# Optimization experiments

Hardware: AMD Instinct MI355X
Metric: run time of the kernel (lower is better)

## Reference

```python
import jax, jax.numpy as jnp
import numpy as np

B, T, D = 4, 2048, 1024
H, DH = 16, 64

def setup_inputs() -> dict:
    key = jax.random.key(0)
    k1, k2, k3 = jax.random.split(key, 3)
    x = jax.random.normal(k1, (B, T, D), dtype=jnp.float32)
    # nn.Linear weights stored [out, in]; we keep that convention
    w_attn = jax.random.normal(k2, (3 * D, D), dtype=jnp.float32) * (1.0 / np.sqrt(D))
    w_proj = jax.random.normal(k3, (D, D), dtype=jnp.float32) * (1.0 / np.sqrt(D))
    return {"x": x, "w_attn": w_attn, "w_proj": w_proj}

def reference(x, w_attn, w_proj):
    Bx, Tx, Dx = x.shape
    qkv = jnp.einsum('btd,ed->bte', x, w_attn)            # [B,T,3D]
    qkv = qkv.reshape(Bx, Tx, 3, H, DH)
    q = qkv[:, :, 0].transpose(0, 2, 1, 3)                # [B,H,T,DH]
    k = qkv[:, :, 1].transpose(0, 2, 1, 3)
    v = qkv[:, :, 2].transpose(0, 2, 1, 3)
    scale = 1.0 / np.sqrt(DH).astype(np.float32)
    att = jnp.einsum('bhqd,bhkd->bhqk', q, k) * scale     # [B,H,T,T]
    causal = jnp.tril(jnp.ones((Tx, Tx), dtype=bool))
    att = jnp.where(causal[None, None], att, jnp.float32(-jnp.inf))
    att = jax.nn.softmax(att, axis=-1)
    y = jnp.einsum('bhqk,bhkd->bhqd', att, v)             # [B,H,T,DH]
    y = y.transpose(0, 2, 1, 3).reshape(Bx, Tx, Dx)       # [B,T,D]
    y = jnp.einsum('btd,ed->bte', y, w_proj)
    return y
```

## Files before the change

### kernel.cpp

```cpp
#include <hip/hip_runtime.h>

typedef unsigned short u16;
typedef __bf16 bf16x8 __attribute__((ext_vector_type(8)));
typedef float floatx4 __attribute__((ext_vector_type(4)));
typedef u16 u16x4 __attribute__((ext_vector_type(4)));

__device__ inline u16 f2bf(float x) {
    __bf16 b = (__bf16)x;
    return __builtin_bit_cast(u16, b);
}

__device__ inline floatx4 fzero() {
    floatx4 z = {0.f, 0.f, 0.f, 0.f};
    return z;
}

#if defined(__has_builtin)
#if __has_builtin(__builtin_amdgcn_exp2f)
#define EXP2F(x) __builtin_amdgcn_exp2f(x)
#endif
#endif
#ifndef EXP2F
#define EXP2F(x) exp2f(x)
#endif

template <bool F32>
__device__ inline bf16x8 ld8(const void* base, size_t off) {
    if constexpr (F32) {
        const float* p = (const float*)base + off;
        float4 a = *(const float4*)p;
        float4 b = *(const float4*)(p + 4);
        union { u16 u[8]; bf16x8 v; } t;
        t.u[0] = f2bf(a.x); t.u[1] = f2bf(a.y); t.u[2] = f2bf(a.z); t.u[3] = f2bf(a.w);
        t.u[4] = f2bf(b.x); t.u[5] = f2bf(b.y); t.u[6] = f2bf(b.z); t.u[7] = f2bf(b.w);
        return t.v;
    } else {
        return *(const bf16x8*)((const u16*)base + off);
    }
}

typedef __attribute__((address_space(1))) const unsigned int as1_u32;
typedef __attribute__((address_space(3))) unsigned int as3_u32;
__device__ inline void gld_lds16(const void* g, void* l) {
    __builtin_amdgcn_global_load_lds((as1_u32*)g, (as3_u32*)l, 16, 0, 0);
}

__device__ inline u16* swz_ptr(u16* buf, int row, int col) {
    return (u16*)((char*)buf + row * 128 + ((col * 2) ^ ((row & 7) << 4)));
}

__global__ __launch_bounds__(256) void cvt_all(const float* __restrict__ x,
                                               const float* __restrict__ wa,
                                               const float* __restrict__ wp,
                                               u16* __restrict__ dst) {
    const int XB8 = 1048576, WAB8 = 393216;
    int i = blockIdx.x * 256 + threadIdx.x;
    const float* src; size_t off;
    if (i < XB8)             { src = x;  off = (size_t)i * 8; }
    else if (i < XB8 + WAB8) { src = wa; off = (size_t)(i - XB8) * 8; }
    else                     { src = wp; off = (size_t)(i - XB8 - WAB8) * 8; }
    *(bf16x8*)(dst + (size_t)i * 8) = ld8<true>(src, off);
}

#define BK 32

template <bool AF32, bool BF32, bool CF32, bool WVT>
__global__ __launch_bounds__(256) void gemm_bt(const void* __restrict__ Ap,
                                               const void* __restrict__ Bp,
                                               void* __restrict__ Cp,
                                               u16* __restrict__ vtp,
                                               int M, int N, int K) {
    __shared__ alignas(16) u16 As[2][128 * BK];
    __shared__ alignas(16) u16 Bs[2][128 * BK];

    const int tid  = threadIdx.x;
    const int lane = tid & 63;
    const int wave = tid >> 6;
    const int wm = (wave >> 1) * 64;
    const int wn = (wave & 1) * 64;
    const int tm = blockIdx.y * 128;
    const int tn = blockIdx.x * 128;
    const int l15 = lane & 15;
    const int l4  = lane >> 4;

    const int srow = tid >> 2;
    const int scol = (tid & 3) * 8;

    floatx4 acc[4][4];
#pragma unroll
    for (int i = 0; i < 4; i++)
#pragma unroll
        for (int j = 0; j < 4; j++) acc[i][j] = fzero();

    if constexpr (!AF32 && !BF32) {
        const u16* Ag = (const u16*)Ap + (size_t)(tm + srow) * K + scol;
        const u16* Bg = (const u16*)Bp + (size_t)(tn + srow) * K + scol;

        auto stage = [&](int buf, int k0) {
            gld_lds16(Ag + k0,                  &As[buf][wave * 512]);
            gld_lds16(Ag + k0 + (size_t)64 * K, &As[buf][2048 + wave * 512]);
            gld_lds16(Bg + k0,                  &Bs[buf][wave * 512]);
            gld_lds16(Bg + k0 + (size_t)64 * K, &Bs[buf][2048 + wave * 512]);
        };

        stage(0, 0);
        __syncthreads();
        int cur = 0;
        const int nk = K / BK;
        for (int t = 0; t < nk; t++) {
            if (t + 1 < nk) stage(cur ^ 1, (t + 1) * BK);

            bf16x8 af[4], bfv[4];
#pragma unroll
            for (int i = 0; i < 4; i++)
                af[i] = *(const bf16x8*)&As[cur][(wm + i * 16 + l15) * BK + l4 * 8];
#pragma unroll
            for (int j = 0; j < 4; j++)
                bfv[j] = *(const bf16x8*)&Bs[cur][(wn + j * 16 + l15) * BK + l4 * 8];
#pragma unroll
            for (int i = 0; i < 4; i++)
#pragma unroll
                for (int j = 0; j < 4; j++)
                    acc[i][j] = __builtin_amdgcn_mfma_f32_16x16x32_bf16(af[i], bfv[j], acc[i][j], 0, 0, 0);

            __syncthreads();
            cur ^= 1;
        }
    } else {
        for (int k0 = 0; k0 < K; k0 += BK) {
            bf16x8 av[2], bv[2];
#pragma unroll
            for (int q = 0; q < 2; q++) {
                av[q] = ld8<AF32>(Ap, (size_t)(tm + srow + q * 64) * K + k0 + scol);
                bv[q] = ld8<BF32>(Bp, (size_t)(tn + srow + q * 64) * K + k0 + scol);
            }
            __syncthreads();
#pragma unroll
            for (int q = 0; q < 2; q++) {
                *(bf16x8*)&As[0][(srow + q * 64) * BK + scol] = av[q];
                *(bf16x8*)&Bs[0][(srow + q * 64) * BK + scol] = bv[q];
            }
            __syncthreads();

            bf16x8 af[4], bfv[4];
#pragma unroll
            for (int i = 0; i < 4; i++)
                af[i] = *(const bf16x8*)&As[0][(wm + i * 16 + l15) * BK + l4 * 8];
#pragma unroll
            for (int j = 0; j < 4; j++)
                bfv[j] = *(const bf16x8*)&Bs[0][(wn + j * 16 + l15) * BK + l4 * 8];
#pragma unroll
            for (int i = 0; i < 4; i++)
#pragma unroll
                for (int j = 0; j < 4; j++)
                    acc[i][j] = __builtin_amdgcn_mfma_f32_16x16x32_bf16(af[i], bfv[j], acc[i][j], 0, 0, 0);
        }
    }

#pragma unroll
    for (int i = 0; i < 4; i++)
#pragma unroll
        for (int j = 0; j < 4; j++) {
            if constexpr (CF32) {
#pragma unroll
                for (int r = 0; r < 4; r++) {
                    int row = tm + wm + i * 16 + l4 * 4 + r;
                    int col = tn + wn + j * 16 + l15;
                    ((float*)Cp)[(size_t)row * N + col] = acc[i][j][r];
                }
            } else {
                u16 v4[4];
#pragma unroll
                for (int r = 0; r < 4; r++) v4[r] = f2bf(acc[i][j][r]);
#pragma unroll
                for (int r = 0; r < 4; r++) {
                    int row = tm + wm + i * 16 + l4 * 4 + r;
                    int col = tn + wn + j * 16 + l15;
                    ((u16*)Cp)[(size_t)row * N + col] = v4[r];
                }
                if constexpr (WVT) {
                    if (tn >= 2048) {
                        int row0 = tm + wm + i * 16 + l4 * 4;
                        int colv = tn + wn + j * 16 + l15 - 2048;
                        int bh = (row0 >> 11) * 16 + (colv >> 6);
                        int dh = colv & 63;
                        int t  = row0 & 2047;
                        u16x4 w = {v4[0], v4[1], v4[2], v4[3]};
                        *(u16x4*)&vtp[(size_t)bh * 131072 + (size_t)dh * 2048 + t] = w;
                    }
                }
            }
        }
}

template <bool USE_VT>
__global__ __launch_bounds__(256) void attn2(const u16* __restrict__ qkv,
                                             const u16* __restrict__ vT,
                                             u16* __restrict__ y) {
    const int T = 2048, CW = 3072;
    __shared__ alignas(16) u16 KP[64 * 64];
    __shared__ alignas(16) u16 Vt[64 * 64];
    __shared__ alignas(16) u16 PB[64 * 64];

    const int tid  = threadIdx.x;
    const int lane = tid & 63;
    const int wave = tid >> 6;
    const int l15 = lane & 15;
    const int l4  = lane >> 4;

    const int bh = blockIdx.x;
    const int qt = 31 - blockIdx.y;
    const int b = bh >> 4, h = bh & 15;
    const int q0 = qt * 64;

    const size_t base = (size_t)b * T * CW + h * 64;
    const u16* qp = qkv + base;
    const u16* kp = qkv + base + 1024;
    const u16* vp = qkv + base + 2048;
    const u16* vtp = USE_VT ? (vT + (size_t)bh * 131072) : nullptr;

    bf16x8 qf[2];
    {
        int qrow = q0 + wave * 16 + l15;
        qf[0] = *(const bf16x8*)&qp[(size_t)qrow * CW + l4 * 8];
        qf[1] = *(const bf16x8*)&qp[(size_t)qrow * CW + 32 + l4 * 8];
    }

    bf16x8 ones;
#pragma unroll
    for (int i = 0; i < 8; i++) ones[i] = (__bf16)1.0f;

    const float C2 = 0.18033688f;
    floatx4 Lacc = fzero();
    floatx4 Oacc[4];
#pragma unroll
    for (int cf = 0; cf < 4; cf++) Oacc[cf] = fzero();

    const int sr = tid >> 3;
    const int sc = tid & 7;

    bf16x8 kreg[2], vreg[2];
    auto stage_load = [&](int kt) {
        const int t0 = kt * 64;
#pragma unroll
        for (int p = 0; p < 2; p++)
            kreg[p] = *(const bf16x8*)&kp[(size_t)(t0 + sr + p * 32) * CW + sc * 8];
        if constexpr (USE_VT) {
#pragma unroll
            for (int p = 0; p < 2; p++)
                vreg[p] = *(const bf16x8*)&vtp[(size_t)(sr + p * 32) * 2048 + t0 + sc * 8];
        } else {
            const int dh = tid & 63;
            const int tb = wave * 8;
#pragma unroll
            for (int p = 0; p < 2; p++) {
                union { u16 u[8]; bf16x8 v; } tmp;
#pragma unroll
                for (int i = 0; i < 8; i++)
                    tmp.u[i] = vp[(size_t)(t0 + tb + p * 32 + i) * CW + dh];
                vreg[p] = tmp.v;
            }
        }
    };

    stage_load(0);

    for (int kt = 0; kt <= qt; kt++) {
        const int t0 = kt * 64;
        __syncthreads();

#pragma unroll
        for (int p = 0; p < 2; p++)
            *(bf16x8*)swz_ptr(KP, sr + p * 32, sc * 8) = kreg[p];
        if constexpr (USE_VT) {
#pragma unroll
            for (int p = 0; p < 2; p++)
                *(bf16x8*)swz_ptr(Vt, sr + p * 32, sc * 8) = vreg[p];
        } else {
            const int dh = tid & 63;
            const int tb = wave * 8;
#pragma unroll
            for (int p = 0; p < 2; p++)
                *(bf16x8*)swz_ptr(Vt, dh, tb + p * 32) = vreg[p];
        }
        __syncthreads();

        if (kt < qt) stage_load(kt + 1);

#pragma unroll
        for (int j = 0; j < 4; j++) {
            bf16x8 k0f = *(const bf16x8*)swz_ptr(KP, j * 16 + l15, l4 * 8);
            bf16x8 k1f = *(const bf16x8*)swz_ptr(KP, j * 16 + l15, 32 + l4 * 8);
            floatx4 s = fzero();
            s = __builtin_amdgcn_mfma_f32_16x16x32_bf16(qf[0], k0f, s, 0, 0, 0);
            s = __builtin_amdgcn_mfma_f32_16x16x32_bf16(qf[1], k1f, s, 0, 0, 0);
            float pj[4];
            if (kt == qt) {
#pragma unroll
                for (int r = 0; r < 4; r++) {
                    int qrow = q0 + wave * 16 + l4 * 4 + r;
                    int krow = t0 + j * 16 + l15;
                    float e = (krow <= qrow) ? s[r] * C2 : -1.0e30f;
                    pj[r] = EXP2F(e);
                }
            } else {
#pragma unroll
                for (int r = 0; r < 4; r++) pj[r] = EXP2F(s[r] * C2);
            }
#pragma unroll
            for (int r = 0; r < 4; r++)
                *swz_ptr(PB, wave * 16 + l4 * 4 + r, j * 16 + l15) = f2bf(pj[r]);
        }

        bf16x8 pf0 = *(const bf16x8*)swz_ptr(PB, wave * 16 + l15, l4 * 8);
        bf16x8 pf1 = *(const bf16x8*)swz_ptr(PB, wave * 16 + l15, 32 + l4 * 8);
        Lacc = __builtin_amdgcn_mfma_f32_16x16x32_bf16(pf0, ones, Lacc, 0, 0, 0);
        Lacc = __builtin_amdgcn_mfma_f32_16x16x32_bf16(pf1, ones, Lacc, 0, 0, 0);
#pragma unroll
        for (int cf = 0; cf < 4; cf++) {
            bf16x8 v0f = *(const bf16x8*)swz_ptr(Vt, cf * 16 + l15, l4 * 8);
            bf16x8 v1f = *(const bf16x8*)swz_ptr(Vt, cf * 16 + l15, 32 + l4 * 8);
            Oacc[cf] = __builtin_amdgcn_mfma_f32_16x16x32_bf16(pf0, v0f, Oacc[cf], 0, 0, 0);
            Oacc[cf] = __builtin_amdgcn_mfma_f32_16x16x32_bf16(pf1, v1f, Oacc[cf], 0, 0, 0);
        }
    }

#pragma unroll
    for (int r = 0; r < 4; r++) {
        float inv = 1.0f / Lacc[r];
        int qrow = q0 + wave * 16 + l4 * 4 + r;
        size_t orow = ((size_t)b * T + qrow) * 1024 + h * 64;
#pragma unroll
        for (int cf = 0; cf < 4; cf++)
            y[orow + cf * 16 + l15] = f2bf(Oacc[cf][r] * inv);
    }
}

extern "C" void kernel_launch(void* const* d_in, const int* in_sizes, int n_in,
                              void* d_out, int out_size, void* d_ws, size_t ws_size,
                              hipStream_t stream) {
    const float* x      = (const float*)d_in[0];
    const float* w_attn = (const float*)d_in[1];
    const float* w_proj = (const float*)d_in[2];
    float* out = (float*)d_out;

    const size_t QKV = (size_t)8192 * 3072;
    const size_t Y   = (size_t)8192 * 1024;
    const size_t VTE = (size_t)64 * 64 * 2048;
    const size_t XB  = (size_t)8192 * 1024;
    const size_t WAB = (size_t)3072 * 1024;
    const size_t WPB = (size_t)1024 * 1024;

    u16* qkv = (u16*)d_ws;
    u16* yb  = qkv + QKV;

    const bool full = ws_size >= (QKV + Y + VTE + XB + WAB + WPB) * sizeof(u16);
    if (ws_size < (QKV + Y) * sizeof(u16)) return;

    dim3 blk(256);
    dim3 g1(3072 / 128, 8192 / 128), g2(1024 / 128, 8192 / 128);
    dim3 ga(64, 32);

    if (full) {
        u16* vT  = yb + Y;
        u16* xb  = vT + VTE;
        cvt_all<<<6144, blk, 0, stream>>>(x, w_attn, w_proj, xb);
        u16* wab = xb + XB;
        u16* wpb = wab + WAB;
        gemm_bt<false, false, false, true><<<g1, blk, 0, stream>>>(xb, wab, qkv, vT, 8192, 3072, 1024);
        attn2<true><<<ga, blk, 0, stream>>>(qkv, vT, yb);
        gemm_bt<false, false, true, false><<<g2, blk, 0, stream>>>(yb, wpb, out, nullptr, 8192, 1024, 1024);
    } else {
        gemm_bt<true, true, false, false><<<g1, blk, 0, stream>>>(x, w_attn, qkv, nullptr, 8192, 3072, 1024);
        attn2<false><<<ga, blk, 0, stream>>>(qkv, nullptr, yb);
        gemm_bt<false, true, true, false><<<g2, blk, 0, stream>>>(yb, w_proj, out, nullptr, 8192, 1024, 1024);
    }
}
```

Before: 255.6 us.

## Split attention waves into 2x2 query/key grid with causal sub-tile skipping

Replaces the attention kernel so each wave handles 32 query rows by 32 keys instead of 16 query rows by all 64 keys. Each loaded K/V fragment is then reused across two query sub-blocks, and waves whose key half lies entirely above the causal diagonal skip their MFMAs. At the end the two key-half partial O and L accumulators are combined through shared memory. This costs an extra reduction pass and two more barriers at the end, plus more accumulator registers per wave. The non-transposed-V fallback path is kept as a separate non-templated kernel.

```diff
diff --git a/kernel.cpp b/kernel.cpp
--- a/kernel.cpp
+++ b/kernel.cpp
@@ -193,10 +193,173 @@
         }
 }
 
-template <bool USE_VT>
-__global__ __launch_bounds__(256) void attn2(const u16* __restrict__ qkv,
+__global__ __launch_bounds__(256) void attn4(const u16* __restrict__ qkv,
                                              const u16* __restrict__ vT,
                                              u16* __restrict__ y) {
+    const int T = 2048, CW = 3072;
+    __shared__ alignas(16) u16 SMEM[3 * 64 * 64];
+    u16* KP = SMEM;
+    u16* Vt = SMEM + 4096;
+    u16* PB = SMEM + 8192;
+
+    const int tid  = threadIdx.x;
+    const int lane = tid & 63;
+    const int wave = tid >> 6;
+    const int wq = wave >> 1;
+    const int wk = wave & 1;
+    const int l15 = lane & 15;
+    const int l4  = lane >> 4;
+
+    const int bh = blockIdx.x;
+    const int qt = 31 - blockIdx.y;
+    const int b = bh >> 4, h = bh & 15;
+    const int q0 = qt * 64;
+    const int qlo = q0 + wq * 32;
+
+    const size_t base = (size_t)b * T * CW + h * 64;
+    const u16* qp = qkv + base;
+    const u16* kp = qkv + base + 1024;
+    const u16* vtp = vT + (size_t)bh * 131072;
+
+    bf16x8 qf[2][2];
+#pragma unroll
+    for (int qb = 0; qb < 2; qb++) {
+        int qrow = qlo + qb * 16 + l15;
+        qf[qb][0] = *(const bf16x8*)&qp[(size_t)qrow * CW + l4 * 8];
+        qf[qb][1] = *(const bf16x8*)&qp[(size_t)qrow * CW + 32 + l4 * 8];
+    }
+
+    bf16x8 ones;
+#pragma unroll
+    for (int i = 0; i < 8; i++) ones[i] = (__bf16)1.0f;
+
+    const float C2 = 0.18033688f;
+    floatx4 Lacc[2] = {fzero(), fzero()};
+    floatx4 Oacc[2][4];
+#pragma unroll
+    for (int qb = 0; qb < 2; qb++)
+#pragma unroll
+        for (int cf = 0; cf < 4; cf++) Oacc[qb][cf] = fzero();
+
+    const int sr = tid >> 3;
+    const int sc = tid & 7;
+
+    bf16x8 kreg[2], vreg[2];
+    auto stage_load = [&](int kt) {
+        const int t0 = kt * 64;
+#pragma unroll
+        for (int p = 0; p < 2; p++)
+            kreg[p] = *(const bf16x8*)&kp[(size_t)(t0 + sr + p * 32) * CW + sc * 8];
+#pragma unroll
+        for (int p = 0; p < 2; p++)
+            vreg[p] = *(const bf16x8*)&vtp[(size_t)(sr + p * 32) * 2048 + t0 + sc * 8];
+    };
+
+    stage_load(0);
+
+    for (int kt = 0; kt <= qt; kt++) {
+        const int t0 = kt * 64;
+        __syncthreads();
+
+#pragma unroll
+        for (int p = 0; p < 2; p++)
+            *(bf16x8*)swz_ptr(KP, sr + p * 32, sc * 8) = kreg[p];
+#pragma unroll
+        for (int p = 0; p < 2; p++)
+            *(bf16x8*)swz_ptr(Vt, sr + p * 32, sc * 8) = vreg[p];
+        __syncthreads();
+
+        if (kt < qt) stage_load(kt + 1);
+
+        const int kbase = t0 + wk * 32;
+        if (kbase <= qlo + 31) {
+            bf16x8 kf[2][2];
+#pragma unroll
+            for (int kb = 0; kb < 2; kb++) {
+                kf[kb][0] = *(const bf16x8*)swz_ptr(KP, wk * 32 + kb * 16 + l15, l4 * 8);
+                kf[kb][1] = *(const bf16x8*)swz_ptr(KP, wk * 32 + kb * 16 + l15, 32 + l4 * 8);
+            }
+            const bool fast = (t0 + 63 <= qlo);
+#pragma unroll
+            for (int qb = 0; qb < 2; qb++)
+#pragma unroll
+                for (int kb = 0; kb < 2; kb++) {
+                    floatx4 s = fzero();
+                    s = __builtin_amdgcn_mfma_f32_16x16x32_bf16(qf[qb][0], kf[kb][0], s, 0, 0, 0);
+                    s = __builtin_amdgcn_mfma_f32_16x16x32_bf16(qf[qb][1], kf[kb][1], s, 0, 0, 0);
+                    float pj[4];
+                    if (fast) {
+#pragma unroll
+                        for (int r = 0; r < 4; r++) pj[r] = EXP2F(s[r] * C2);
+                    } else {
+#pragma unroll
+                        for (int r = 0; r < 4; r++) {
+                            int qrow = qlo + qb * 16 + l4 * 4 + r;
+                            int krow = kbase + kb * 16 + l15;
+                            float e = (krow <= qrow) ? s[r] * C2 : -1.0e30f;
+                            pj[r] = EXP2F(e);
+                        }
+                    }
+#pragma unroll
+                    for (int r = 0; r < 4; r++)
+                        *swz_ptr(PB, wq * 32 + qb * 16 + l4 * 4 + r,
+                                 wk * 32 + kb * 16 + l15) = f2bf(pj[r]);
+                }
+
+            bf16x8 pf[2];
+#pragma unroll
+            for (int qb = 0; qb < 2; qb++) {
+                pf[qb] = *(const bf16x8*)swz_ptr(PB, wq * 32 + qb * 16 + l15, wk * 32 + l4 * 8);
+                Lacc[qb] = __builtin_amdgcn_mfma_f32_16x16x32_bf16(pf[qb], ones, Lacc[qb], 0, 0, 0);
+            }
+#pragma unroll
+            for (int cf = 0; cf < 4; cf++) {
+                bf16x8 vb = *(const bf16x8*)swz_ptr(Vt, cf * 16 + l15, wk * 32 + l4 * 8);
+#pragma unroll
+                for (int qb = 0; qb < 2; qb++)
+                    Oacc[qb][cf] = __builtin_amdgcn_mfma_f32_16x16x32_bf16(pf[qb], vb, Oacc[qb][cf], 0, 0, 0);
+            }
+        }
+    }
+
+    __syncthreads();
+    float* Obuf = (float*)SMEM;
+    float* Lbuf = (float*)(SMEM + 8192);
+    if (wk == 1) {
+#pragma unroll
+        for (int qb = 0; qb < 2; qb++)
+#pragma unroll
+            for (int cf = 0; cf < 4; cf++)
+#pragma unroll
+                for (int r = 0; r < 4; r++)
+                    Obuf[(wq * 32 + qb * 16 + l4 * 4 + r) * 64 + cf * 16 + l15] = Oacc[qb][cf][r];
+        if (l15 == 0)
+#pragma unroll
+            for (int qb = 0; qb < 2; qb++)
+#pragma unroll
+                for (int r = 0; r < 4; r++)
+                    Lbuf[wq * 32 + qb * 16 + l4 * 4 + r] = Lacc[qb][r];
+    }
+    __syncthreads();
+    if (wk == 0) {
+#pragma unroll
+        for (int qb = 0; qb < 2; qb++)
+#pragma unroll
+            for (int r = 0; r < 4; r++) {
+                int qr = wq * 32 + qb * 16 + l4 * 4 + r;
+                float inv = 1.0f / (Lacc[qb][r] + Lbuf[qr]);
+                size_t orow = ((size_t)b * T + q0 + qr) * 1024 + h * 64;
+#pragma unroll
+                for (int cf = 0; cf < 4; cf++) {
+                    float o = Oacc[qb][cf][r] + Obuf[qr * 64 + cf * 16 + l15];
+                    y[orow + cf * 16 + l15] = f2bf(o * inv);
+                }
+            }
+    }
+}
+
+__global__ __launch_bounds__(256) void attn2f(const u16* __restrict__ qkv,
+                                              u16* __restrict__ y) {
     const int T = 2048, CW = 3072;
     __shared__ alignas(16) u16 KP[64 * 64];
     __shared__ alignas(16) u16 Vt[64 * 64];
@@ -217,7 +380,6 @@
     const u16* qp = qkv + base;
     const u16* kp = qkv + base + 1024;
     const u16* vp = qkv + base + 2048;
-    const u16* vtp = USE_VT ? (vT + (size_t)bh * 131072) : nullptr;
 
     bf16x8 qf[2];
     {
@@ -245,21 +407,15 @@
 #pragma unroll
         for (int p = 0; p < 2; p++)
             kreg[p] = *(const bf16x8*)&kp[(size_t)(t0 + sr + p * 32) * CW + sc * 8];
-        if constexpr (USE_VT) {
-#pragma unroll
-            for (int p = 0; p < 2; p++)
-                vreg[p] = *(const bf16x8*)&vtp[(size_t)(sr + p * 32) * 2048 + t0 + sc * 8];
-        } else {
-            const int dh = tid & 63;
-            const int tb = wave * 8;
-#pragma unroll
-            for (int p = 0; p < 2; p++) {
-                union { u16 u[8]; bf16x8 v; } tmp;
-#pragma unroll
-                for (int i = 0; i < 8; i++)
-                    tmp.u[i] = vp[(size_t)(t0 + tb + p * 32 + i) * CW + dh];
-                vreg[p] = tmp.v;
-            }
+        const int dh = tid & 63;
+        const int tb = wave * 8;
+#pragma unroll
+        for (int p = 0; p < 2; p++) {
+            union { u16 u[8]; bf16x8 v; } tmp;
+#pragma unroll
+            for (int i = 0; i < 8; i++)
+                tmp.u[i] = vp[(size_t)(t0 + tb + p * 32 + i) * CW + dh];
+            vreg[p] = tmp.v;
         }
     };
 
@@ -268,15 +424,10 @@
     for (int kt = 0; kt <= qt; kt++) {
         const int t0 = kt * 64;
         __syncthreads();
-
 #pragma unroll
         for (int p = 0; p < 2; p++)
             *(bf16x8*)swz_ptr(KP, sr + p * 32, sc * 8) = kreg[p];
-        if constexpr (USE_VT) {
-#pragma unroll
-            for (int p = 0; p < 2; p++)
-                *(bf16x8*)swz_ptr(Vt, sr + p * 32, sc * 8) = vreg[p];
-        } else {
+        {
             const int dh = tid & 63;
             const int tb = wave * 8;
 #pragma unroll
@@ -368,11 +519,11 @@
         u16* wab = xb + XB;
         u16* wpb = wab + WAB;
         gemm_bt<false, false, false, true><<<g1, blk, 0, stream>>>(xb, wab, qkv, vT, 8192, 3072, 1024);
-        attn2<true><<<ga, blk, 0, stream>>>(qkv, vT, yb);
+        attn4<<<ga, blk, 0, stream>>>(qkv, vT, yb);
         gemm_bt<false, false, true, false><<<g2, blk, 0, stream>>>(yb, wpb, out, nullptr, 8192, 1024, 1024);
     } else {
         gemm_bt<true, true, false, false><<<g1, blk, 0, stream>>>(x, w_attn, qkv, nullptr, 8192, 3072, 1024);
-        attn2<false><<<ga, blk, 0, stream>>>(qkv, nullptr, yb);
+        attn2f<<<ga, blk, 0, stream>>>(qkv, yb);
         gemm_bt<false, true, true, false><<<g2, blk, 0, stream>>>(yb, w_proj, out, nullptr, 8192, 1024, 1024);
     }
 }
```

Result: slower. 273.6 us (+7.0%).
